# Optimization experiments

Measured on AMD Instinct MI355X. Metric: run time of the kernel, lower is better.

Reference implementation:

```python
import jax, jax.numpy as jnp
import numpy as np

B, H, W, C_IN, F = 4, 64, 64, 128, 256


def setup_inputs() -> dict:
    key = jax.random.key(0)
    ks = jax.random.split(key, 6)
    return {
        "inputs": jax.random.normal(ks[0], (B, H, W, C_IN), dtype=jnp.float32),
        "W_proj": jax.random.normal(ks[1], (C_IN, F), dtype=jnp.float32) * 0.02,
        "b_proj": jnp.zeros((F,), dtype=jnp.float32),
        "W_q": jax.random.normal(ks[2], (F, F), dtype=jnp.float32) * 0.02,
        "b_q": jnp.zeros((F,), dtype=jnp.float32),
        "W_k": jax.random.normal(ks[3], (F, F), dtype=jnp.float32) * 0.02,
        "b_k": jnp.zeros((F,), dtype=jnp.float32),
        "W_v": jax.random.normal(ks[4], (F, F), dtype=jnp.float32) * 0.02,
        "b_v": jnp.zeros((F,), dtype=jnp.float32),
        "gamma": jax.random.uniform(ks[5], (1,), dtype=jnp.float32),
    }


def reference(inputs, W_proj, b_proj, W_q, b_q, W_k, b_k, W_v, b_v, gamma):
    # 1x1 conv projection (C_in -> filters) since input channels != filters
    x = jnp.einsum("bhwc,cf->bhwf", inputs, W_proj) + b_proj  # [B,H,W,F]
    q = jnp.einsum("bhwf,fg->bhwg", x, W_q) + b_q
    k = jnp.einsum("bhwf,fg->bhwg", x, W_k) + b_k
    v = jnp.einsum("bhwf,fg->bhwg", x, W_v) + b_v
    b, h, w, f = x.shape
    n = h * w
    qr = q.reshape(b, n, f)
    kr = k.reshape(b, n, f)
    vr = v.reshape(b, n, f)
    attn = jax.nn.softmax(jnp.einsum("bnf,bmf->bnm", qr, kr), axis=-1)  # [B,N,N]
    context = jnp.einsum("bnm,bmf->bnf", attn, vr).reshape(b, h, w, f)
    return gamma * context + x
```

## Files before the change

### kernel.cpp

```cpp
#include <hip/hip_runtime.h>
#include <hip/hip_bf16.h>
#include <stdint.h>

typedef __attribute__((ext_vector_type(8))) short short8;
typedef __attribute__((ext_vector_type(4))) float floatx4;
typedef __attribute__((ext_vector_type(16))) float floatx16;
typedef __attribute__((ext_vector_type(2))) long longx2;

#define DEVI __device__ __forceinline__
#define MFMA16(a, b, c) __builtin_amdgcn_mfma_f32_16x16x32_bf16((a), (b), (c), 0, 0, 0)
#define MFMA32(a, b, c) __builtin_amdgcn_mfma_f32_32x32x16_fp8_fp8((a), (b), (c), 0, 0, 0)

typedef __attribute__((address_space(3))) unsigned int lds_u32;
typedef __attribute__((address_space(1))) const unsigned int glb_u32;
#define GLOAD_LDS16(g, l) __builtin_amdgcn_global_load_lds((glb_u32*)(g), (lds_u32*)(l), 16, 0, 0)

DEVI unsigned short f2bf(float x) {
    union { float f; unsigned int u; } v; v.f = x;
    unsigned int r = v.u + 0x7FFFu + ((v.u >> 16) & 1u);
    return (unsigned short)(r >> 16);
}
DEVI float bf2f(unsigned short h) {
    union { unsigned int u; float f; } v; v.u = ((unsigned int)h) << 16;
    return v.f;
}
DEVI unsigned char f2fp8(float x) {
    int c = __builtin_amdgcn_cvt_pk_fp8_f32(x, x, 0, false);
    return (unsigned char)(c & 0xFF);
}

__global__ __launch_bounds__(256) void prep_weights(
    const float* __restrict__ Wp, const float* __restrict__ Wq,
    const float* __restrict__ Wk, const float* __restrict__ Wv,
    unsigned short* __restrict__ Tp, unsigned short* __restrict__ Tq,
    unsigned short* __restrict__ Tk, unsigned short* __restrict__ Tv)
{
    int idx = blockIdx.x * blockDim.x + threadIdx.x;
    if (idx < 32768) {
        int k = idx >> 8, n = idx & 255;
        Tp[n * 128 + k] = f2bf(Wp[idx]);
    } else {
        int r = idx - 32768;
        int m = r >> 16, i = r & 65535;
        const float* W   = (m == 0) ? Wq : (m == 1) ? Wk : Wv;
        unsigned short* T = (m == 0) ? Tq : (m == 1) ? Tk : Tv;
        int k = i >> 8, n = i & 255;
        T[n * 256 + k] = f2bf(W[i]);
    }
}


__global__ __launch_bounds__(256) void gemm_bias(
    const float* __restrict__ A,
    const unsigned short* __restrict__ Wt,
    const float* __restrict__ bias,
    unsigned short* __restrict__ Cb,
    int N)
{
    __shared__ __align__(16) unsigned short As[64][136];
    __shared__ __align__(16) unsigned short Bs[64][136];
    const int tid  = threadIdx.x;
    const int w    = tid >> 6;
    const int lane = tid & 63;
    const int quad = lane >> 4;
    const int l15  = lane & 15;
    const int m0 = blockIdx.x * 64;
    const int n0 = blockIdx.y * 64;

    floatx4 acc[4];
    #pragma unroll
    for (int t = 0; t < 4; ++t) acc[t] = (floatx4)0.0f;

    #pragma unroll
    for (int it = 0; it < 8; ++it) {
        int idx = tid + it * 256;
        int r = idx >> 5, c4 = idx & 31;
        float4 v = *(const float4*)&A[(size_t)(m0 + r) * 128 + c4 * 4];
        ushort4 o;
        o.x = f2bf(v.x); o.y = f2bf(v.y); o.z = f2bf(v.z); o.w = f2bf(v.w);
        *(ushort4*)&As[r][c4 * 4] = o;
    }
    #pragma unroll
    for (int it = 0; it < 4; ++it) {
        int idx = tid + it * 256;
        int r = idx >> 4, g = idx & 15;
        *(short8*)&Bs[r][g * 8] = *(const short8*)&Wt[(size_t)(n0 + r) * 128 + g * 8];
    }
    __syncthreads();
    #pragma unroll
    for (int s = 0; s < 4; ++s) {
        short8 a = *(const short8*)&As[w * 16 + l15][s * 32 + quad * 8];
        #pragma unroll
        for (int t = 0; t < 4; ++t) {
            short8 bfr = *(const short8*)&Bs[t * 16 + l15][s * 32 + quad * 8];
            acc[t] = MFMA16(a, bfr, acc[t]);
        }
    }

    __syncthreads();
    unsigned short* T = &As[0][0];
    #pragma unroll
    for (int t = 0; t < 4; ++t) {
        int n = n0 + t * 16 + l15;
        float bs = bias[n];
        #pragma unroll
        for (int r = 0; r < 4; ++r)
            T[(w * 16 + quad * 4 + r) * 80 + t * 16 + l15] = f2bf(acc[t][r] + bs);
    }
    __syncthreads();
    int row = tid >> 2, c8 = (tid & 3) * 8;
    #pragma unroll
    for (int half = 0; half < 2; ++half) {
        int4 ov = *(const int4*)&T[row * 80 + c8 + half * 32];
        *(int4*)&Cb[(size_t)(m0 + row) * N + n0 + c8 + half * 32] = ov;
    }
}


__global__ __launch_bounds__(256) void gemm_qkv(
    const unsigned short* __restrict__ A,
    const unsigned short* __restrict__ Wt0, const unsigned short* __restrict__ Wt1, const unsigned short* __restrict__ Wt2,
    const float* __restrict__ b0, const float* __restrict__ b1, const float* __restrict__ b2,
    unsigned char* __restrict__ C0, unsigned char* __restrict__ C1, unsigned char* __restrict__ C2,
    int N)
{
    const unsigned short* Wt = (blockIdx.z == 0) ? Wt0 : (blockIdx.z == 1) ? Wt1 : Wt2;
    const float* bias        = (blockIdx.z == 0) ? b0  : (blockIdx.z == 1) ? b1  : b2;
    unsigned char* Cb        = (blockIdx.z == 0) ? C0  : (blockIdx.z == 1) ? C1  : C2;

    __shared__ __align__(16) unsigned short As[64][136];
    __shared__ __align__(16) unsigned short Bs[64][136];
    const int tid  = threadIdx.x;
    const int w    = tid >> 6;
    const int lane = tid & 63;
    const int quad = lane >> 4;
    const int l15  = lane & 15;
    const int m0 = blockIdx.x * 64;
    const int n0 = blockIdx.y * 64;

    floatx4 acc[4];
    #pragma unroll
    for (int t = 0; t < 4; ++t) acc[t] = (floatx4)0.0f;

    for (int kc = 0; kc < 256; kc += 128) {
        __syncthreads();
        #pragma unroll
        for (int idx = tid; idx < 1024; idx += 256) {
            int r = idx >> 4, g = idx & 15;
            *(short8*)&As[r][g * 8] = *(const short8*)&A[(size_t)(m0 + r) * 256 + kc + g * 8];
            *(short8*)&Bs[r][g * 8] = *(const short8*)&Wt[(size_t)(n0 + r) * 256 + kc + g * 8];
        }
        __syncthreads();
        #pragma unroll
        for (int s = 0; s < 4; ++s) {
            short8 a = *(const short8*)&As[w * 16 + l15][s * 32 + quad * 8];
            #pragma unroll
            for (int t = 0; t < 4; ++t) {
                short8 bfr = *(const short8*)&Bs[t * 16 + l15][s * 32 + quad * 8];
                acc[t] = MFMA16(a, bfr, acc[t]);
            }
        }
    }

    __syncthreads();
    unsigned char* T = (unsigned char*)&As[0][0];
    #pragma unroll
    for (int t = 0; t < 4; ++t) {
        int n = n0 + t * 16 + l15;
        float bs = bias[n];
        #pragma unroll
        for (int r = 0; r < 4; ++r)
            T[(w * 16 + quad * 4 + r) * 80 + t * 16 + l15] = f2fp8(acc[t][r] + bs);
    }
    __syncthreads();

    const int b  = m0 >> 12;
    const int mt = (m0 & 4095) >> 5;

    if (blockIdx.z == 0) {
        int row = tid >> 2, c16 = (tid & 3) * 16;
        int4 vq = *(const int4*)&T[row * 80 + c16];
        *(int4*)&Cb[(size_t)(m0 + row) * 256 + n0 + c16] = vq;
    } else {
        const int kt  = tid >> 7;
        const int sub = (tid >> 6) & 1;
        const int ln  = tid & 63;
        const int l31b = ln & 31, hib = ln >> 5;
        union { long h[2]; int4 v; unsigned char bts[16]; } o;
        if (blockIdx.z == 1) {
            #pragma unroll
            for (int h = 0; h < 2; ++h)
                o.h[h] = *(const long*)&T[(kt * 32 + l31b) * 80 + (sub * 2 + h) * 16 + hib * 8];
        } else {
            #pragma unroll
            for (int s2 = 0; s2 < 2; ++s2)
                #pragma unroll
                for (int j = 0; j < 8; ++j)
                    o.bts[s2 * 8 + j] = T[(kt * 32 + s2 * 16 + hib * 8 + j) * 80 + sub * 32 + l31b];
        }
        unsigned char* dst = Cb + (size_t)b * 1048576 + (size_t)(mt + kt) * 8192
                           + (size_t)((n0 >> 5) + sub) * 1024 + ln * 16;
        *(int4*)dst = o.v;
    }
}


__global__ __launch_bounds__(512, 2) void flash_attn(
    const unsigned char* __restrict__ qg,
    const unsigned char* __restrict__ kp,
    const unsigned char* __restrict__ vp,
    const unsigned short* __restrict__ xb,
    const float* __restrict__ gamma,
    float* __restrict__ out)
{
    __shared__ __align__(16) unsigned char KV[2][65536];
    float* MbF = (float*)&KV[0][0];
    float* Ml  = MbF + 64 * 264;

    const int tid  = threadIdx.x;
    const int w    = tid >> 6;
    const int lane = tid & 63;
    const int l31  = lane & 31;
    const int hi   = lane >> 5;
    const int kq   = w & 3;
    const int rw   = w >> 2;
    const int blk  = blockIdx.x;
    const int b    = (blk & 7) >> 1;
    const int rt   = (blk >> 3) * 2 + (blk & 1);
    const int row0 = rt * 64 + rw * 32;

    const size_t baseQ = ((size_t)b * 4096 + row0 + l31) * 256 + hi * 8;
    long qf[16];
    #pragma unroll
    for (int s = 0; s < 16; ++s)
        qf[s] = *(const long*)&qg[baseQ + s * 16];

    const long ones8 = 0x3838383838383838L;

    floatx16 ctx[8];
    #pragma unroll
    for (int i = 0; i < 8; ++i) ctx[i] = (floatx16)0.0f;
    floatx16 lacc = (floatx16)0.0f;

    const unsigned char* kb_b = kp + (size_t)b * 1048576;
    const unsigned char* vb_b = vp + (size_t)b * 1048576;

#define FA_STAGE(T, BUF)                                                             \
    {                                                                                \
        _Pragma("unroll")                                                            \
        for (int p = 0; p < 8; ++p) {                                                \
            const int c    = p * 8 + w;                                              \
            const int ckq  = c >> 4;                                                 \
            const int csel = (c >> 3) & 1;                                           \
            const int coff = (c & 7) * 1024;                                         \
            const unsigned char* src = (csel ? vb_b : kb_b)                          \
                + (size_t)ckq * 262144 + (size_t)(T) * 8192 + coff + lane * 16;      \
            GLOAD_LDS16(src, &KV[BUF][ckq * 16384 + csel * 8192 + coff]);            \
        }                                                                            \
    }

    FA_STAGE(0, 0)

    for (int t = 0; t < 32; ++t) {
        const int buf = t & 1;
        __syncthreads();
        if (t < 31) FA_STAGE(t + 1, buf ^ 1)

        const unsigned char* kc = &KV[buf][kq * 16384];
        const unsigned char* vc = &KV[buf][kq * 16384 + 8192];

        longx2 kk[8];
        #pragma unroll
        for (int p = 0; p < 8; ++p)
            kk[p] = *(const longx2*)&kc[p * 1024 + lane * 16];
        floatx16 sa = (floatx16)0.0f, sb = (floatx16)0.0f;
        __builtin_amdgcn_s_setprio(1);
        #pragma unroll
        for (int p = 0; p < 8; ++p) {
            sa = MFMA32(kk[p].x, qf[2 * p],     sa);
            sb = MFMA32(kk[p].y, qf[2 * p + 1], sb);
        }
        __builtin_amdgcn_s_setprio(0);

        float e[16];
        #pragma unroll
        for (int r = 0; r < 16; ++r) e[r] = __expf(sa[r] + sb[r]);
        int X0 = __builtin_amdgcn_cvt_pk_fp8_f32(e[0],  e[1],  0,  false);
        X0     = __builtin_amdgcn_cvt_pk_fp8_f32(e[2],  e[3],  X0, true);
        int Y0 = __builtin_amdgcn_cvt_pk_fp8_f32(e[4],  e[5],  0,  false);
        Y0     = __builtin_amdgcn_cvt_pk_fp8_f32(e[6],  e[7],  Y0, true);
        int X1 = __builtin_amdgcn_cvt_pk_fp8_f32(e[8],  e[9],  0,  false);
        X1     = __builtin_amdgcn_cvt_pk_fp8_f32(e[10], e[11], X1, true);
        int Y1 = __builtin_amdgcn_cvt_pk_fp8_f32(e[12], e[13], 0,  false);
        Y1     = __builtin_amdgcn_cvt_pk_fp8_f32(e[14], e[15], Y1, true);
        asm volatile("v_permlane32_swap_b32 %0, %1" : "+v"(X0), "+v"(Y0));
        asm volatile("v_permlane32_swap_b32 %0, %1" : "+v"(X1), "+v"(Y1));
        union { int i2[2]; long l; } u0, u1;
        u0.i2[0] = X0; u0.i2[1] = Y0;
        u1.i2[0] = X1; u1.i2[1] = Y1;
        const long ap0 = u0.l;
        const long ap1 = u1.l;

        lacc = MFMA32(ap0, ones8, lacc);
        lacc = MFMA32(ap1, ones8, lacc);
        __builtin_amdgcn_s_setprio(1);
        #pragma unroll
        for (int p = 0; p < 8; ++p) {
            longx2 vv = *(const longx2*)&vc[p * 1024 + lane * 16];
            ctx[p] = MFMA32(ap0, vv.x, ctx[p]);
            ctx[p] = MFMA32(ap1, vv.y, ctx[p]);
        }
        __builtin_amdgcn_s_setprio(0);
    }
#undef FA_STAGE

    __syncthreads();
    for (int pass = 3; pass >= 0; --pass) {
        if (kq == pass) {
            #pragma unroll
            for (int fb = 0; fb < 8; ++fb) {
                #pragma unroll
                for (int r = 0; r < 16; ++r) {
                    int row = rw * 32 + (r & 3) + 8 * (r >> 2) + 4 * hi;
                    int idx = row * 264 + fb * 32 + l31;
                    float prev = (pass == 3) ? 0.0f : MbF[idx];
                    MbF[idx] = prev + ctx[fb][r];
                }
            }
            if (l31 == 0) {
                #pragma unroll
                for (int r = 0; r < 16; ++r) {
                    int row = rw * 32 + (r & 3) + 8 * (r >> 2) + 4 * hi;
                    float prev = (pass == 3) ? 0.0f : Ml[row];
                    Ml[row] = prev + lacc[r];
                }
            }
        }
        __syncthreads();
    }

    const float g = gamma[0];
    const int row = tid >> 3;
    const int c0  = (tid & 7) * 32;
    const float rl = 1.0f / Ml[row];
    const size_t o = ((size_t)b * 4096 + rt * 64 + row) * 256 + c0;
    #pragma unroll
    for (int j = 0; j < 4; ++j) {
        short8 xv = *(const short8*)&xb[o + j * 8];
        float res[8];
        #pragma unroll
        for (int i = 0; i < 8; ++i)
            res[i] = g * MbF[row * 264 + c0 + j * 8 + i] * rl + bf2f((unsigned short)xv[i]);
        *(float4*)&out[o + j * 8]     = *(float4*)&res[0];
        *(float4*)&out[o + j * 8 + 4] = *(float4*)&res[4];
    }
}


extern "C" void kernel_launch(void* const* d_in, const int* in_sizes, int n_in,
                              void* d_out, int out_size, void* d_ws, size_t ws_size,
                              hipStream_t stream)
{
    const float* inp   = (const float*)d_in[0];
    const float* Wp    = (const float*)d_in[1];
    const float* bp    = (const float*)d_in[2];
    const float* Wq    = (const float*)d_in[3];
    const float* bq    = (const float*)d_in[4];
    const float* Wk    = (const float*)d_in[5];
    const float* bk    = (const float*)d_in[6];
    const float* Wv    = (const float*)d_in[7];
    const float* bv    = (const float*)d_in[8];
    const float* gamma = (const float*)d_in[9];
    float* out = (float*)d_out;

    char* ws = (char*)d_ws;
    unsigned char*  q8    = (unsigned char*)(ws + 0);
    unsigned char*  k8    = (unsigned char*)(ws + 4194304);
    unsigned char*  v8    = (unsigned char*)(ws + 8388608);
    unsigned short* x_b   = (unsigned short*)(ws + 12582912);
    unsigned short* Wt_p  = (unsigned short*)(ws + 20971520);
    unsigned short* Wt_q  = (unsigned short*)(ws + 21037056);
    unsigned short* Wt_k  = (unsigned short*)(ws + 21168128);
    unsigned short* Wt_v  = (unsigned short*)(ws + 21299200);

    prep_weights<<<896, 256, 0, stream>>>(Wp, Wq, Wk, Wv, Wt_p, Wt_q, Wt_k, Wt_v);
    gemm_bias<<<dim3(256, 4), 256, 0, stream>>>(inp, Wt_p, bp, x_b, 256);
    gemm_qkv<<<dim3(256, 4, 3), 256, 0, stream>>>(x_b, Wt_q, Wt_k, Wt_v, bq, bk, bv,
                                                  q8, k8, v8, 256);
    flash_attn<<<256, 512, 0, stream>>>(q8, k8, v8, x_b, gamma, out);
}
```

Measured before the change: 190.4 us.

## Fuse weight prep into GEMMs and split attention loop into barrier-separated phases

Removes the separate prep_weights launch. Both projection GEMMs now read the fp32 weights directly, converting to bf16 and transposing into shared memory on the fly. This drops one kernel launch and the workspace round-trip, at the cost of redundant conversion per block and strided scalar LDS stores. The flash attention main loop is split into half-stage phases separated by explicit s_barriers, interleaving next-tile async K/V loads with the current QK and PV MFMA work so waves stay in lockstep. The extra barriers add sync cost.

Measured after the change: 205.2 us. 7.8% more time.

```diff
diff --git a/kernel.cpp b/kernel.cpp
--- a/kernel.cpp
+++ b/kernel.cpp
@@ -29,30 +29,10 @@
     return (unsigned char)(c & 0xFF);
 }
 
-__global__ __launch_bounds__(256) void prep_weights(
-    const float* __restrict__ Wp, const float* __restrict__ Wq,
-    const float* __restrict__ Wk, const float* __restrict__ Wv,
-    unsigned short* __restrict__ Tp, unsigned short* __restrict__ Tq,
-    unsigned short* __restrict__ Tk, unsigned short* __restrict__ Tv)
-{
-    int idx = blockIdx.x * blockDim.x + threadIdx.x;
-    if (idx < 32768) {
-        int k = idx >> 8, n = idx & 255;
-        Tp[n * 128 + k] = f2bf(Wp[idx]);
-    } else {
-        int r = idx - 32768;
-        int m = r >> 16, i = r & 65535;
-        const float* W   = (m == 0) ? Wq : (m == 1) ? Wk : Wv;
-        unsigned short* T = (m == 0) ? Tq : (m == 1) ? Tk : Tv;
-        int k = i >> 8, n = i & 255;
-        T[n * 256 + k] = f2bf(W[i]);
-    }
-}
-
 
 __global__ __launch_bounds__(256) void gemm_bias(
     const float* __restrict__ A,
-    const unsigned short* __restrict__ Wt,
+    const float* __restrict__ Wp,
     const float* __restrict__ bias,
     unsigned short* __restrict__ Cb,
     int N)
@@ -81,10 +61,14 @@
         *(ushort4*)&As[r][c4 * 4] = o;
     }
     #pragma unroll
-    for (int it = 0; it < 4; ++it) {
-        int idx = tid + it * 256;
-        int r = idx >> 4, g = idx & 15;
-        *(short8*)&Bs[r][g * 8] = *(const short8*)&Wt[(size_t)(n0 + r) * 128 + g * 8];
+    for (int it = 0; it < 8; ++it) {
+        int flat = tid + it * 256;
+        int k = flat >> 4, n4 = flat & 15;
+        float4 v = *(const float4*)&Wp[(size_t)k * 256 + n0 + n4 * 4];
+        Bs[n4 * 4 + 0][k] = f2bf(v.x);
+        Bs[n4 * 4 + 1][k] = f2bf(v.y);
+        Bs[n4 * 4 + 2][k] = f2bf(v.z);
+        Bs[n4 * 4 + 3][k] = f2bf(v.w);
     }
     __syncthreads();
     #pragma unroll
@@ -119,14 +103,14 @@
 
 __global__ __launch_bounds__(256) void gemm_qkv(
     const unsigned short* __restrict__ A,
-    const unsigned short* __restrict__ Wt0, const unsigned short* __restrict__ Wt1, const unsigned short* __restrict__ Wt2,
+    const float* __restrict__ W0, const float* __restrict__ W1, const float* __restrict__ W2,
     const float* __restrict__ b0, const float* __restrict__ b1, const float* __restrict__ b2,
     unsigned char* __restrict__ C0, unsigned char* __restrict__ C1, unsigned char* __restrict__ C2,
     int N)
 {
-    const unsigned short* Wt = (blockIdx.z == 0) ? Wt0 : (blockIdx.z == 1) ? Wt1 : Wt2;
-    const float* bias        = (blockIdx.z == 0) ? b0  : (blockIdx.z == 1) ? b1  : b2;
-    unsigned char* Cb        = (blockIdx.z == 0) ? C0  : (blockIdx.z == 1) ? C1  : C2;
+    const float* W    = (blockIdx.z == 0) ? W0 : (blockIdx.z == 1) ? W1 : W2;
+    const float* bias = (blockIdx.z == 0) ? b0 : (blockIdx.z == 1) ? b1 : b2;
+    unsigned char* Cb = (blockIdx.z == 0) ? C0 : (blockIdx.z == 1) ? C1 : C2;
 
     __shared__ __align__(16) unsigned short As[64][136];
     __shared__ __align__(16) unsigned short Bs[64][136];
@@ -148,7 +132,16 @@
         for (int idx = tid; idx < 1024; idx += 256) {
             int r = idx >> 4, g = idx & 15;
             *(short8*)&As[r][g * 8] = *(const short8*)&A[(size_t)(m0 + r) * 256 + kc + g * 8];
-            *(short8*)&Bs[r][g * 8] = *(const short8*)&Wt[(size_t)(n0 + r) * 256 + kc + g * 8];
+        }
+        #pragma unroll
+        for (int it = 0; it < 8; ++it) {
+            int flat = tid + it * 256;
+            int k = flat >> 4, n4 = flat & 15;
+            float4 v = *(const float4*)&W[(size_t)(kc + k) * 256 + n0 + n4 * 4];
+            Bs[n4 * 4 + 0][k] = f2bf(v.x);
+            Bs[n4 * 4 + 1][k] = f2bf(v.y);
+            Bs[n4 * 4 + 2][k] = f2bf(v.z);
+            Bs[n4 * 4 + 3][k] = f2bf(v.w);
         }
         __syncthreads();
         #pragma unroll
@@ -245,10 +238,10 @@
     const unsigned char* kb_b = kp + (size_t)b * 1048576;
     const unsigned char* vb_b = vp + (size_t)b * 1048576;
 
-#define FA_STAGE(T, BUF)                                                             \
+#define FA_STAGE_H(T, BUF, PH)                                                       \
     {                                                                                \
         _Pragma("unroll")                                                            \
-        for (int p = 0; p < 8; ++p) {                                                \
+        for (int p = (PH) * 4; p < (PH) * 4 + 4; ++p) {                              \
             const int c    = p * 8 + w;                                              \
             const int ckq  = c >> 4;                                                 \
             const int csel = (c >> 3) & 1;                                           \
@@ -258,30 +251,50 @@
             GLOAD_LDS16(src, &KV[BUF][ckq * 16384 + csel * 8192 + coff]);            \
         }                                                                            \
     }
-
-    FA_STAGE(0, 0)
+#define PHASE_BAR asm volatile("s_barrier" ::: "memory")
+
+    FA_STAGE_H(0, 0, 0) FA_STAGE_H(0, 0, 1)
 
     for (int t = 0; t < 32; ++t) {
         const int buf = t & 1;
         __syncthreads();
-        if (t < 31) FA_STAGE(t + 1, buf ^ 1)
 
         const unsigned char* kc = &KV[buf][kq * 16384];
-        const unsigned char* vc = &KV[buf][kq * 16384 + 8192];
-
-        longx2 kk[8];
-        #pragma unroll
-        for (int p = 0; p < 8; ++p)
-            kk[p] = *(const longx2*)&kc[p * 1024 + lane * 16];
+        const unsigned char* vc = kc + 8192;
+
         floatx16 sa = (floatx16)0.0f, sb = (floatx16)0.0f;
+
+        longx2 k0[4];
+        #pragma unroll
+        for (int p = 0; p < 4; ++p) k0[p] = *(const longx2*)&kc[p * 1024 + lane * 16];
+        if (t < 31) FA_STAGE_H(t + 1, buf ^ 1, 0)
+        PHASE_BAR;
         __builtin_amdgcn_s_setprio(1);
         #pragma unroll
-        for (int p = 0; p < 8; ++p) {
-            sa = MFMA32(kk[p].x, qf[2 * p],     sa);
-            sb = MFMA32(kk[p].y, qf[2 * p + 1], sb);
+        for (int p = 0; p < 4; ++p) {
+            sa = MFMA32(k0[p].x, qf[2 * p],     sa);
+            sb = MFMA32(k0[p].y, qf[2 * p + 1], sb);
         }
         __builtin_amdgcn_s_setprio(0);
-
+        PHASE_BAR;
+
+        longx2 k1[4];
+        #pragma unroll
+        for (int p = 0; p < 4; ++p) k1[p] = *(const longx2*)&kc[(4 + p) * 1024 + lane * 16];
+        if (t < 31) FA_STAGE_H(t + 1, buf ^ 1, 1)
+        PHASE_BAR;
+        __builtin_amdgcn_s_setprio(1);
+        #pragma unroll
+        for (int p = 0; p < 4; ++p) {
+            sa = MFMA32(k1[p].x, qf[2 * (4 + p)],     sa);
+            sb = MFMA32(k1[p].y, qf[2 * (4 + p) + 1], sb);
+        }
+        __builtin_amdgcn_s_setprio(0);
+        PHASE_BAR;
+
+        longx2 v0[4];
+        #pragma unroll
+        for (int p = 0; p < 4; ++p) v0[p] = *(const longx2*)&vc[p * 1024 + lane * 16];
         float e[16];
         #pragma unroll
         for (int r = 0; r < 16; ++r) e[r] = __expf(sa[r] + sb[r]);
@@ -300,19 +313,32 @@
         u1.i2[0] = X1; u1.i2[1] = Y1;
         const long ap0 = u0.l;
         const long ap1 = u1.l;
-
+        PHASE_BAR;
+        __builtin_amdgcn_s_setprio(1);
         lacc = MFMA32(ap0, ones8, lacc);
         lacc = MFMA32(ap1, ones8, lacc);
+        #pragma unroll
+        for (int p = 0; p < 4; ++p) {
+            ctx[p] = MFMA32(ap0, v0[p].x, ctx[p]);
+            ctx[p] = MFMA32(ap1, v0[p].y, ctx[p]);
+        }
+        __builtin_amdgcn_s_setprio(0);
+        PHASE_BAR;
+
+        longx2 v1[4];
+        #pragma unroll
+        for (int p = 0; p < 4; ++p) v1[p] = *(const longx2*)&vc[(4 + p) * 1024 + lane * 16];
+        PHASE_BAR;
         __builtin_amdgcn_s_setprio(1);
         #pragma unroll
-        for (int p = 0; p < 8; ++p) {
-            longx2 vv = *(const longx2*)&vc[p * 1024 + lane * 16];
-            ctx[p] = MFMA32(ap0, vv.x, ctx[p]);
-            ctx[p] = MFMA32(ap1, vv.y, ctx[p]);
+        for (int p = 0; p < 4; ++p) {
+            ctx[4 + p] = MFMA32(ap0, v1[p].x, ctx[4 + p]);
+            ctx[4 + p] = MFMA32(ap1, v1[p].y, ctx[4 + p]);
         }
         __builtin_amdgcn_s_setprio(0);
     }
-#undef FA_STAGE
+#undef FA_STAGE_H
+#undef PHASE_BAR
 
     __syncthreads();
     for (int pass = 3; pass >= 0; --pass) {
@@ -378,14 +404,9 @@
     unsigned char*  k8    = (unsigned char*)(ws + 4194304);
     unsigned char*  v8    = (unsigned char*)(ws + 8388608);
     unsigned short* x_b   = (unsigned short*)(ws + 12582912);
-    unsigned short* Wt_p  = (unsigned short*)(ws + 20971520);
-    unsigned short* Wt_q  = (unsigned short*)(ws + 21037056);
-    unsigned short* Wt_k  = (unsigned short*)(ws + 21168128);
-    unsigned short* Wt_v  = (unsigned short*)(ws + 21299200);
-
-    prep_weights<<<896, 256, 0, stream>>>(Wp, Wq, Wk, Wv, Wt_p, Wt_q, Wt_k, Wt_v);
-    gemm_bias<<<dim3(256, 4), 256, 0, stream>>>(inp, Wt_p, bp, x_b, 256);
-    gemm_qkv<<<dim3(256, 4, 3), 256, 0, stream>>>(x_b, Wt_q, Wt_k, Wt_v, bq, bk, bv,
+
+    gemm_bias<<<dim3(256, 4), 256, 0, stream>>>(inp, Wp, bp, x_b, 256);
+    gemm_qkv<<<dim3(256, 4, 3), 256, 0, stream>>>(x_b, Wq, Wk, Wv, bq, bk, bv,
                                                   q8, k8, v8, 256);
     flash_attn<<<256, 512, 0, stream>>>(q8, k8, v8, x_b, gamma, out);
 }
```
